# Kernel tuning notes

Measured on AMD Instinct MI355X. Metric: run time of the kernel, lower is better.

## Reference

```python
import jax, jax.numpy as jnp
import numpy as np

NEG = -1e30

def leaky_relu(x, slope=0.2):
    return jnp.where(x >= 0, x, slope * x)

def setup_inputs() -> dict:
    key = jax.random.key(0)
    ks = jax.random.split(key, 6)
    N, E, R, D, H = 50000, 640000, 4, 256, 128
    x = jax.random.normal(ks[0], (N, D), dtype=jnp.float32)
    edge_index = jax.random.randint(ks[1], (2, E), 0, N, dtype=jnp.int64)
    edge_type = jax.random.randint(ks[2], (E,), 0, R, dtype=jnp.int64)
    a = jax.random.normal(ks[3], (1, 2 * H, 1), dtype=jnp.float32) * 0.1
    W = jax.random.normal(ks[4], (R, D, H), dtype=jnp.float32) * (1.0 / np.sqrt(D))
    b = jax.random.normal(ks[5], (R, H), dtype=jnp.float32) * 0.01
    return {"x": x, "edge_index": edge_index, "edge_type": edge_type, "a": a, "W": W, "b": b}

def reference(x, edge_index, edge_type, a, W, b):
    # eval mode: both dropouts are identity
    N = x.shape[0]
    R, _, H = W.shape
    row, col = edge_index[0], edge_index[1]
    att = a[0][:, 0]           # [2H]
    a1, a2 = att[:H], att[H:]  # split of concat([h_row, h_col]) @ a
    out = jnp.zeros((N, H), dtype=x.dtype)
    for r in range(R):
        h = x @ W[r] + b[r]                 # [N, H]
        h_row = h[row]                      # [E, H] gather
        h_col = h[col]                      # [E, H] gather
        e = leaky_relu(h_row @ a1 + h_col @ a2)  # [E]
        mask = edge_type == r
        # segment softmax over destination `row`, restricted to this relation
        e_m = jnp.where(mask, e, NEG)
        seg_max = jax.ops.segment_max(e_m, row, num_segments=N)  # [N]
        seg_max = jnp.where(seg_max < 0.5 * NEG, 0.0, seg_max)
        w = jnp.where(mask, jnp.exp(e - seg_max[row]), 0.0)      # [E]
        seg_sum = jax.ops.segment_sum(w, row, num_segments=N)    # [N]
        denom = jnp.where(seg_sum > 0, seg_sum, 1.0)
        alpha = w / denom[row]                                   # [E]
        out = out + jnp.zeros((N, H), dtype=x.dtype).at[row].add(h_col * alpha[:, None])
    return out
```

## Files before the change

kernel.cpp:

```cpp
#include <hip/hip_runtime.h>
#include <hip/hip_bf16.h>

#define D_DIM 256
#define H_DIM 128
#define R_DIM 4
#define SLOTS 64

typedef __bf16 bf16x8 __attribute__((ext_vector_type(8)));
typedef float f32x4 __attribute__((ext_vector_type(4)));

__device__ __forceinline__ unsigned short f2bf(float f) {
    union { float f; unsigned u; } v; v.f = f;
    unsigned r = (v.u + 0x7FFFu + ((v.u >> 16) & 1u)) >> 16;
    return (unsigned short)r;
}
__device__ __forceinline__ float bflo(unsigned v) {
    union { unsigned u; float f; } w; w.u = v << 16; return w.f;
}
__device__ __forceinline__ float bfhi(unsigned v) {
    union { unsigned u; float f; } w; w.u = v & 0xFFFF0000u; return w.f;
}

__global__ void __launch_bounds__(256)
kprep_kernel(const float* __restrict__ W, const float* __restrict__ b,
             const float* __restrict__ a,
             float* __restrict__ v1, float* __restrict__ v2,
             float* __restrict__ c1, float* __restrict__ c2,
             unsigned short* __restrict__ Wt, int* __restrict__ cnt, int N) {
    int idx = blockIdx.x * 256 + threadIdx.x;
    {
        int d = idx & 255;
        int h = (idx >> 8) & 127;
        int r = idx >> 15;
        Wt[idx] = f2bf(W[((size_t)(r * D_DIM + d)) * H_DIM + h]);
    }
    if (idx < N) cnt[idx] = 0;
    if (idx < R_DIM * D_DIM) {
        int r = idx >> 8;
        int d = idx & 255;
        const float* wp = W + ((size_t)r * D_DIM + d) * H_DIM;
        float acc1 = 0.f, acc2 = 0.f;
        for (int h = 0; h < H_DIM; ++h) {
            float w = wp[h];
            acc1 += w * a[h];
            acc2 += w * a[H_DIM + h];
        }
        v1[idx] = acc1; v2[idx] = acc2;
    }
    if (idx < R_DIM) {
        const float* bp = b + idx * H_DIM;
        float acc1 = 0.f, acc2 = 0.f;
        for (int h = 0; h < H_DIM; ++h) {
            acc1 += bp[h] * a[h];
            acc2 += bp[h] * a[H_DIM + h];
        }
        c1[idx] = acc1; c2[idx] = acc2;
    }
}

#define A_BYTES (128 * 512)
#define BSLOT_BYTES (128 * 64)
__global__ void __launch_bounds__(512)
kmain_kernel(const float* __restrict__ x, const unsigned short* __restrict__ Wt,
             const float* __restrict__ bias, __hip_bfloat16* __restrict__ Hall,
             const int* __restrict__ eidx, const int* __restrict__ etype,
             const float* __restrict__ v1, const float* __restrict__ v2,
             const float* __restrict__ c1, const float* __restrict__ c2,
             float* __restrict__ s1, float* __restrict__ s2,
             int* __restrict__ cnt, unsigned* recs4,
             int N, int E, int GB, int KB) {
    __shared__ __align__(16) char lds[A_BYTES + 2 * BSLOT_BYTES];
    const int bid = (int)blockIdx.x;
    const int t = threadIdx.x;

    if (bid < GB) {
        const int lane = t & 63;
        const int w = t >> 6;
        const int wm = w >> 2;
        const int wn = w & 3;
        const int q = lane >> 4;
        const int l15 = lane & 15;
        const int nBase = bid * 128;
        const int hB = t >> 2, hCh = t & 3;

        uint4 aR[8];
        #pragma unroll
        for (int i = 0; i < 8; ++i) {
            int idx = i * 512 + t;
            int n = idx >> 5, ch = idx & 31;
            int gn = nBase + n; if (gn >= N) gn = N - 1;
            const float4* xp = (const float4*)(x + (size_t)gn * D_DIM + ch * 8);
            float4 va = xp[0], vb = xp[1];
            aR[i].x = (unsigned)f2bf(va.x) | ((unsigned)f2bf(va.y) << 16);
            aR[i].y = (unsigned)f2bf(va.z) | ((unsigned)f2bf(va.w) << 16);
            aR[i].z = (unsigned)f2bf(vb.x) | ((unsigned)f2bf(vb.y) << 16);
            aR[i].w = (unsigned)f2bf(vb.z) | ((unsigned)f2bf(vb.w) << 16);
        }
        uint4 bR = *(const uint4*)(Wt + (size_t)hB * D_DIM + hCh * 8);
        #pragma unroll
        for (int i = 0; i < 8; ++i) {
            int idx = i * 512 + t;
            int n = idx >> 5, ch = idx & 31;
            *(uint4*)(lds + n * 512 + ((ch ^ (n & 7)) << 4)) = aR[i];
        }
        *(uint4*)(lds + A_BYTES + hB * 64 + ((hCh ^ ((hB >> 1) & 3)) << 4)) = bR;
        __syncthreads();

        f32x4 acc[2][4];
        {
            #pragma unroll
            for (int hf = 0; hf < 2; ++hf) {
                f32x4 bv = *(const f32x4*)(bias + 0 * H_DIM + wn * 32 + hf * 16 + q * 4);
                #pragma unroll
                for (int nf = 0; nf < 4; ++nf) acc[hf][nf] = bv;
            }
        }

        int cur = 0;
        #pragma unroll 1
        for (int c = 0; c < 32; ++c) {
            const int r = c >> 3;
            uint4 nb;
            if (c < 31) {
                int cn = c + 1;
                nb = *(const uint4*)(Wt + ((size_t)((cn >> 3) * H_DIM + hB)) * D_DIM + (cn & 7) * 32 + hCh * 8);
            }
            bf16x8 wf[2], xf[4];
            #pragma unroll
            for (int hf = 0; hf < 2; ++hf) {
                int hl = wn * 32 + hf * 16 + l15;
                wf[hf] = *(const bf16x8*)(lds + A_BYTES + (cur ? BSLOT_BYTES : 0) + hl * 64 + ((q ^ ((hl >> 1) & 3)) << 4));
            }
            #pragma unroll
            for (int nf = 0; nf < 4; ++nf) {
                int nl = wm * 64 + nf * 16 + l15;
                int sA = ((c & 7) << 2) | q;
                xf[nf] = *(const bf16x8*)(lds + nl * 512 + ((sA ^ (nl & 7)) << 4));
            }
            #pragma unroll
            for (int hf = 0; hf < 2; ++hf)
                #pragma unroll
                for (int nf = 0; nf < 4; ++nf)
                    acc[hf][nf] = __builtin_amdgcn_mfma_f32_16x16x32_bf16(wf[hf], xf[nf], acc[hf][nf], 0, 0, 0);
            if (c < 31)
                *(uint4*)(lds + A_BYTES + (cur ? 0 : BSLOT_BYTES) + hB * 64 + ((hCh ^ ((hB >> 1) & 3)) << 4)) = nb;
            __syncthreads();
            cur ^= 1;
            if ((c & 7) == 7) {
                #pragma unroll
                for (int hf = 0; hf < 2; ++hf) {
                    int h = wn * 32 + hf * 16 + q * 4;
                    #pragma unroll
                    for (int nf = 0; nf < 4; ++nf) {
                        int n = nBase + wm * 64 + nf * 16 + l15;
                        if (n < N) {
                            unsigned lo = (unsigned)f2bf(acc[hf][nf][0]) | ((unsigned)f2bf(acc[hf][nf][1]) << 16);
                            unsigned hi = (unsigned)f2bf(acc[hf][nf][2]) | ((unsigned)f2bf(acc[hf][nf][3]) << 16);
                            *(uint2*)((unsigned short*)Hall + ((size_t)r * N + n) * H_DIM + h) = make_uint2(lo, hi);
                        }
                    }
                }
                if (c < 31) {
                    #pragma unroll
                    for (int hf = 0; hf < 2; ++hf) {
                        f32x4 bv = *(const f32x4*)(bias + (r + 1) * H_DIM + wn * 32 + hf * 16 + q * 4);
                        #pragma unroll
                        for (int nf = 0; nf < 4; ++nf) acc[hf][nf] = bv;
                    }
                }
            }
        }
    } else if (bid < GB + KB) {
        const int kb = bid - GB;
        const int base = kb * 2048 + t;
        int row[4], col[4], rr[4];
        bool ok[4];
        #pragma unroll
        for (int j = 0; j < 4; ++j) {
            int e = base + j * 512;
            ok[j] = (e < E);
            int ee = ok[j] ? e : 0;
            row[j] = eidx[ee];
            col[j] = eidx[E + ee];
            rr[j] = etype[ee];
        }
        int slot[4];
        #pragma unroll
        for (int j = 0; j < 4; ++j)
            slot[j] = ok[j] ? atomicAdd(&cnt[row[j]], 1) : SLOTS;
        #pragma unroll
        for (int j = 0; j < 4; ++j) {
            if (ok[j] && slot[j] < SLOTS) {
                unsigned u = ((unsigned)rr[j] << 28) | (unsigned)(rr[j] * N + col[j]);
                recs4[(size_t)row[j] * 128 + slot[j]] = u;
            }
        }
    } else {
        float* sv1 = (float*)lds;
        float* sv2 = (float*)(lds + 4096);
        float* scs = (float*)(lds + 8192);
        const int sb = bid - GB - KB;
        for (int i = t; i < R_DIM * D_DIM; i += 512) { sv1[i] = v1[i]; sv2[i] = v2[i]; }
        if (t < 4) { scs[t] = c1[t]; scs[4 + t] = c2[t]; }
        __syncthreads();
        const int wave = t >> 6, lane = t & 63;
        const int n = sb * 8 + wave;
        if (n >= N) return;
        float4 xv = *(const float4*)(x + (size_t)n * D_DIM + lane * 4);
        float d0, d1, d2, d3, d4, d5, d6, d7;
        {
            float4 w;
            w = *(const float4*)&sv1[0 * D_DIM + lane * 4]; d0 = xv.x*w.x + xv.y*w.y + xv.z*w.z + xv.w*w.w;
            w = *(const float4*)&sv1[1 * D_DIM + lane * 4]; d1 = xv.x*w.x + xv.y*w.y + xv.z*w.z + xv.w*w.w;
            w = *(const float4*)&sv1[2 * D_DIM + lane * 4]; d2 = xv.x*w.x + xv.y*w.y + xv.z*w.z + xv.w*w.w;
            w = *(const float4*)&sv1[3 * D_DIM + lane * 4]; d3 = xv.x*w.x + xv.y*w.y + xv.z*w.z + xv.w*w.w;
            w = *(const float4*)&sv2[0 * D_DIM + lane * 4]; d4 = xv.x*w.x + xv.y*w.y + xv.z*w.z + xv.w*w.w;
            w = *(const float4*)&sv2[1 * D_DIM + lane * 4]; d5 = xv.x*w.x + xv.y*w.y + xv.z*w.z + xv.w*w.w;
            w = *(const float4*)&sv2[2 * D_DIM + lane * 4]; d6 = xv.x*w.x + xv.y*w.y + xv.z*w.z + xv.w*w.w;
            w = *(const float4*)&sv2[3 * D_DIM + lane * 4]; d7 = xv.x*w.x + xv.y*w.y + xv.z*w.z + xv.w*w.w;
        }
        #pragma unroll
        for (int o = 32; o > 0; o >>= 1) {
            d0 += __shfl_xor(d0, o); d1 += __shfl_xor(d1, o);
            d2 += __shfl_xor(d2, o); d3 += __shfl_xor(d3, o);
            d4 += __shfl_xor(d4, o); d5 += __shfl_xor(d5, o);
            d6 += __shfl_xor(d6, o); d7 += __shfl_xor(d7, o);
        }
        if (lane == 0) {
            s1[(size_t)0 * N + n] = d0 + scs[0];
            s1[(size_t)1 * N + n] = d1 + scs[1];
            s1[(size_t)2 * N + n] = d2 + scs[2];
            s1[(size_t)3 * N + n] = d3 + scs[3];
            s2[(size_t)0 * N + n] = d4 + scs[4];
            s2[(size_t)1 * N + n] = d5 + scs[5];
            s2[(size_t)2 * N + n] = d6 + scs[6];
            s2[(size_t)3 * N + n] = d7 + scs[7];
        }
    }
}

__global__ void __launch_bounds__(256)
krow10_kernel(const unsigned* recs4, const int* __restrict__ cnt,
              const float* __restrict__ s1, const float* __restrict__ s2,
              const __hip_bfloat16* __restrict__ Hall,
              float* out, int N) {
    const int wave = threadIdx.x >> 6;
    const int lane = threadIdx.x & 63;
    const int half = lane >> 5;
    const int l32 = lane & 31;
    const int n = blockIdx.x * 4 + wave;
    if (n >= N) return;
    int deg = cnt[n]; if (deg > SLOTS) deg = SLOTS;
    deg = __builtin_amdgcn_readfirstlane(deg);
    const unsigned* rp = recs4 + (size_t)n * 128;
    const uint2* hp = (const uint2*)Hall;

    unsigned u = rp[(lane < deg) ? lane : 0];
    const unsigned off_l = u & 0x0FFFFFFFu;
    const int r_l = (int)(u >> 28);

    float s1v0 = s1[n], s1v1 = s1[N + n], s1v2 = s1[2 * (size_t)N + n], s1v3 = s1[3 * (size_t)N + n];
    float s2v = 0.f;
    if (lane < deg) s2v = s2[off_l];
    float wgt = 0.f;
    if (lane < deg) {
        float s1sel = (r_l == 0) ? s1v0 : (r_l == 1) ? s1v1 : (r_l == 2) ? s1v2 : s1v3;
        float sc = s1sel + s2v;
        sc = (sc >= 0.f) ? sc : 0.2f * sc;
        wgt = __expf(sc);
    }

    float i0, i1, i2, i3;
    {
        float v0 = (r_l == 0) ? wgt : 0.f;
        float v1 = (r_l == 1) ? wgt : 0.f;
        float v2 = (r_l == 2) ? wgt : 0.f;
        float v3 = (r_l == 3) ? wgt : 0.f;
        #pragma unroll
        for (int o = 32; o > 0; o >>= 1) {
            v0 += __shfl_xor(v0, o);
            v1 += __shfl_xor(v1, o);
            v2 += __shfl_xor(v2, o);
            v3 += __shfl_xor(v3, o);
        }
        i0 = (v0 > 0.f) ? 1.f / v0 : 0.f;
        i1 = (v1 > 0.f) ? 1.f / v1 : 0.f;
        i2 = (v2 > 0.f) ? 1.f / v2 : 0.f;
        i3 = (v3 > 0.f) ? 1.f / v3 : 0.f;
    }
    float alpha = wgt * ((r_l == 0) ? i0 : (r_l == 1) ? i1 : (r_l == 2) ? i2 : i3);

    float a0 = 0.f, a1 = 0.f, a2 = 0.f, a3 = 0.f;
    for (int c0 = 0; c0 < deg; c0 += 16) {
        unsigned offs[8]; float als[8]; uint2 vv[8];
        #pragma unroll
        for (int pp = 0; pp < 8; ++pp) {
            int idx = c0 + pp * 2 + half;
            int src = (idx < deg) ? idx : 0;
            unsigned ux = (unsigned)__shfl((int)off_l, src);
            float av = __shfl(alpha, src);
            als[pp] = (idx < deg) ? av : 0.f;
            offs[pp] = ux;
        }
        #pragma unroll
        for (int pp = 0; pp < 8; ++pp) vv[pp] = hp[(size_t)offs[pp] * 32 + l32];
        #pragma unroll
        for (int pp = 0; pp < 8; ++pp) {
            a0 += als[pp] * bflo(vv[pp].x);
            a1 += als[pp] * bfhi(vv[pp].x);
            a2 += als[pp] * bflo(vv[pp].y);
            a3 += als[pp] * bfhi(vv[pp].y);
        }
    }

    a0 += __shfl_xor(a0, 32);
    a1 += __shfl_xor(a1, 32);
    a2 += __shfl_xor(a2, 32);
    a3 += __shfl_xor(a3, 32);
    if (half == 0)
        *(float4*)(out + (size_t)n * H_DIM + l32 * 4) = make_float4(a0, a1, a2, a3);
}

static inline char* carve(char*& p, size_t bytes) {
    char* q = p;
    p += (bytes + 255) & ~(size_t)255;
    return q;
}

extern "C" void kernel_launch(void* const* d_in, const int* in_sizes, int n_in,
                              void* d_out, int out_size, void* d_ws, size_t ws_size,
                              hipStream_t stream) {
    const float* x     = (const float*)d_in[0];
    const int*   eidx  = (const int*)d_in[1];
    const int*   etype = (const int*)d_in[2];
    const float* a     = (const float*)d_in[3];
    const float* W     = (const float*)d_in[4];
    const float* b     = (const float*)d_in[5];
    float* out = (float*)d_out;

    const int E = in_sizes[2];
    const int N = in_sizes[0] / D_DIM;

    char* p = (char*)d_ws;
    __hip_bfloat16* Hall = (__hip_bfloat16*)carve(p, (size_t)R_DIM * N * H_DIM * 2);
    unsigned short* Wt   = (unsigned short*)carve(p, (size_t)R_DIM * D_DIM * H_DIM * 2);
    float* s1     = (float*)carve(p, (size_t)R_DIM * N * 4);
    float* s2     = (float*)carve(p, (size_t)R_DIM * N * 4);
    float* v1     = (float*)carve(p, R_DIM * D_DIM * 4);
    float* v2     = (float*)carve(p, R_DIM * D_DIM * 4);
    float* c1     = (float*)carve(p, 64);
    float* c2     = (float*)carve(p, 64);
    int*   cnt    = (int*)carve(p, (size_t)N * 4);

    unsigned* recs4 = (unsigned*)d_out;

    kprep_kernel<<<512, 256, 0, stream>>>(W, b, a, v1, v2, c1, c2, Wt, cnt, N);
    const int GB = (N + 127) / 128;
    const int KB = (E + 2047) / 2048;
    const int SB = (N + 7) / 8;
    kmain_kernel<<<GB + KB + SB, 512, 0, stream>>>(x, Wt, b, Hall, eidx, etype,
                                                   v1, v2, c1, c2, s1, s2, cnt, recs4,
                                                   N, E, GB, KB);
    krow10_kernel<<<(N + 3) / 4, 256, 0, stream>>>(recs4, cnt, s1, s2, Hall, out, N);
}
```

Before: 119.8 us.

## Merge score-projection blocks into edge-bucketing blocks with grid-stride loop

The separate score blocks (one per 8 nodes, about 6250 blocks) are removed. The edge-bucketing blocks now also compute the s1/s2 node projections with a grid-stride loop, reading v1/v2/c1/c2 straight from global memory instead of staging them in LDS. The LDS array moves inside the GEMM branch, which may let the compiler assign it only where it is used. This cuts block launch and LDS staging overhead and shrinks the grid, but each remaining block now does much more serial work, which could leave the tail unbalanced.

Result: slower. 132.9 us (+10.9%).

```diff
diff --git a/kernel.cpp b/kernel.cpp
--- a/kernel.cpp
+++ b/kernel.cpp
@@ -69,11 +69,11 @@
              float* __restrict__ s1, float* __restrict__ s2,
              int* __restrict__ cnt, unsigned* recs4,
              int N, int E, int GB, int KB) {
-    __shared__ __align__(16) char lds[A_BYTES + 2 * BSLOT_BYTES];
     const int bid = (int)blockIdx.x;
     const int t = threadIdx.x;
 
     if (bid < GB) {
+        __shared__ __align__(16) char lds[A_BYTES + 2 * BSLOT_BYTES];
         const int lane = t & 63;
         const int w = t >> 6;
         const int wm = w >> 2;
@@ -170,71 +170,70 @@
                 }
             }
         }
-    } else if (bid < GB + KB) {
+    } else {
         const int kb = bid - GB;
-        const int base = kb * 2048 + t;
-        int row[4], col[4], rr[4];
-        bool ok[4];
-        #pragma unroll
-        for (int j = 0; j < 4; ++j) {
-            int e = base + j * 512;
-            ok[j] = (e < E);
-            int ee = ok[j] ? e : 0;
-            row[j] = eidx[ee];
-            col[j] = eidx[E + ee];
-            rr[j] = etype[ee];
-        }
-        int slot[4];
-        #pragma unroll
-        for (int j = 0; j < 4; ++j)
-            slot[j] = ok[j] ? atomicAdd(&cnt[row[j]], 1) : SLOTS;
-        #pragma unroll
-        for (int j = 0; j < 4; ++j) {
-            if (ok[j] && slot[j] < SLOTS) {
-                unsigned u = ((unsigned)rr[j] << 28) | (unsigned)(rr[j] * N + col[j]);
-                recs4[(size_t)row[j] * 128 + slot[j]] = u;
-            }
-        }
-    } else {
-        float* sv1 = (float*)lds;
-        float* sv2 = (float*)(lds + 4096);
-        float* scs = (float*)(lds + 8192);
-        const int sb = bid - GB - KB;
-        for (int i = t; i < R_DIM * D_DIM; i += 512) { sv1[i] = v1[i]; sv2[i] = v2[i]; }
-        if (t < 4) { scs[t] = c1[t]; scs[4 + t] = c2[t]; }
-        __syncthreads();
-        const int wave = t >> 6, lane = t & 63;
-        const int n = sb * 8 + wave;
-        if (n >= N) return;
-        float4 xv = *(const float4*)(x + (size_t)n * D_DIM + lane * 4);
-        float d0, d1, d2, d3, d4, d5, d6, d7;
         {
-            float4 w;
-            w = *(const float4*)&sv1[0 * D_DIM + lane * 4]; d0 = xv.x*w.x + xv.y*w.y + xv.z*w.z + xv.w*w.w;
-            w = *(const float4*)&sv1[1 * D_DIM + lane * 4]; d1 = xv.x*w.x + xv.y*w.y + xv.z*w.z + xv.w*w.w;
-            w = *(const float4*)&sv1[2 * D_DIM + lane * 4]; d2 = xv.x*w.x + xv.y*w.y + xv.z*w.z + xv.w*w.w;
-            w = *(const float4*)&sv1[3 * D_DIM + lane * 4]; d3 = xv.x*w.x + xv.y*w.y + xv.z*w.z + xv.w*w.w;
-            w = *(const float4*)&sv2[0 * D_DIM + lane * 4]; d4 = xv.x*w.x + xv.y*w.y + xv.z*w.z + xv.w*w.w;
-            w = *(const float4*)&sv2[1 * D_DIM + lane * 4]; d5 = xv.x*w.x + xv.y*w.y + xv.z*w.z + xv.w*w.w;
-            w = *(const float4*)&sv2[2 * D_DIM + lane * 4]; d6 = xv.x*w.x + xv.y*w.y + xv.z*w.z + xv.w*w.w;
-            w = *(const float4*)&sv2[3 * D_DIM + lane * 4]; d7 = xv.x*w.x + xv.y*w.y + xv.z*w.z + xv.w*w.w;
-        }
-        #pragma unroll
-        for (int o = 32; o > 0; o >>= 1) {
-            d0 += __shfl_xor(d0, o); d1 += __shfl_xor(d1, o);
-            d2 += __shfl_xor(d2, o); d3 += __shfl_xor(d3, o);
-            d4 += __shfl_xor(d4, o); d5 += __shfl_xor(d5, o);
-            d6 += __shfl_xor(d6, o); d7 += __shfl_xor(d7, o);
-        }
-        if (lane == 0) {
-            s1[(size_t)0 * N + n] = d0 + scs[0];
-            s1[(size_t)1 * N + n] = d1 + scs[1];
-            s1[(size_t)2 * N + n] = d2 + scs[2];
-            s1[(size_t)3 * N + n] = d3 + scs[3];
-            s2[(size_t)0 * N + n] = d4 + scs[4];
-            s2[(size_t)1 * N + n] = d5 + scs[5];
-            s2[(size_t)2 * N + n] = d6 + scs[6];
-            s2[(size_t)3 * N + n] = d7 + scs[7];
+            const int base = kb * 2048 + t;
+            int row[4], col[4], rr[4];
+            bool ok[4];
+            #pragma unroll
+            for (int j = 0; j < 4; ++j) {
+                int e = base + j * 512;
+                ok[j] = (e < E);
+                int ee = ok[j] ? e : 0;
+                row[j] = eidx[ee];
+                col[j] = eidx[E + ee];
+                rr[j] = etype[ee];
+            }
+            int slot[4];
+            #pragma unroll
+            for (int j = 0; j < 4; ++j)
+                slot[j] = ok[j] ? atomicAdd(&cnt[row[j]], 1) : SLOTS;
+            #pragma unroll
+            for (int j = 0; j < 4; ++j) {
+                if (ok[j] && slot[j] < SLOTS) {
+                    unsigned u = ((unsigned)rr[j] << 28) | (unsigned)(rr[j] * N + col[j]);
+                    recs4[(size_t)row[j] * 128 + slot[j]] = u;
+                }
+            }
+        }
+        {
+            const int wave = t >> 6, lane = t & 63;
+            const int rstride = KB * 8;
+            const float4* v1p = (const float4*)v1;
+            const float4* v2p = (const float4*)v2;
+            for (int n = kb * 8 + wave; n < N; n += rstride) {
+                float4 xv = *(const float4*)(x + (size_t)n * D_DIM + lane * 4);
+                float d0, d1, d2, d3, d4, d5, d6, d7;
+                {
+                    float4 w;
+                    w = v1p[(0 * D_DIM >> 2) + lane]; d0 = xv.x*w.x + xv.y*w.y + xv.z*w.z + xv.w*w.w;
+                    w = v1p[(1 * D_DIM >> 2) + lane]; d1 = xv.x*w.x + xv.y*w.y + xv.z*w.z + xv.w*w.w;
+                    w = v1p[(2 * D_DIM >> 2) + lane]; d2 = xv.x*w.x + xv.y*w.y + xv.z*w.z + xv.w*w.w;
+                    w = v1p[(3 * D_DIM >> 2) + lane]; d3 = xv.x*w.x + xv.y*w.y + xv.z*w.z + xv.w*w.w;
+                    w = v2p[(0 * D_DIM >> 2) + lane]; d4 = xv.x*w.x + xv.y*w.y + xv.z*w.z + xv.w*w.w;
+                    w = v2p[(1 * D_DIM >> 2) + lane]; d5 = xv.x*w.x + xv.y*w.y + xv.z*w.z + xv.w*w.w;
+                    w = v2p[(2 * D_DIM >> 2) + lane]; d6 = xv.x*w.x + xv.y*w.y + xv.z*w.z + xv.w*w.w;
+                    w = v2p[(3 * D_DIM >> 2) + lane]; d7 = xv.x*w.x + xv.y*w.y + xv.z*w.z + xv.w*w.w;
+                }
+                #pragma unroll
+                for (int o = 32; o > 0; o >>= 1) {
+                    d0 += __shfl_xor(d0, o); d1 += __shfl_xor(d1, o);
+                    d2 += __shfl_xor(d2, o); d3 += __shfl_xor(d3, o);
+                    d4 += __shfl_xor(d4, o); d5 += __shfl_xor(d5, o);
+                    d6 += __shfl_xor(d6, o); d7 += __shfl_xor(d7, o);
+                }
+                if (lane == 0) {
+                    s1[(size_t)0 * N + n] = d0 + c1[0];
+                    s1[(size_t)1 * N + n] = d1 + c1[1];
+                    s1[(size_t)2 * N + n] = d2 + c1[2];
+                    s1[(size_t)3 * N + n] = d3 + c1[3];
+                    s2[(size_t)0 * N + n] = d4 + c2[0];
+                    s2[(size_t)1 * N + n] = d5 + c2[1];
+                    s2[(size_t)2 * N + n] = d6 + c2[2];
+                    s2[(size_t)3 * N + n] = d7 + c2[3];
+                }
+            }
         }
     }
 }
@@ -357,9 +356,8 @@
     kprep_kernel<<<512, 256, 0, stream>>>(W, b, a, v1, v2, c1, c2, Wt, cnt, N);
     const int GB = (N + 127) / 128;
     const int KB = (E + 2047) / 2048;
-    const int SB = (N + 7) / 8;
-    kmain_kernel<<<GB + KB + SB, 512, 0, stream>>>(x, Wt, b, Hall, eidx, etype,
-                                                   v1, v2, c1, c2, s1, s2, cnt, recs4,
-                                                   N, E, GB, KB);
+    kmain_kernel<<<GB + KB, 512, 0, stream>>>(x, Wt, b, Hall, eidx, etype,
+                                              v1, v2, c1, c2, s1, s2, cnt, recs4,
+                                              N, E, GB, KB);
     krow10_kernel<<<(N + 3) / 4, 256, 0, stream>>>(recs4, cnt, s1, s2, Hall, out, N);
 }
```
